# Optimization experiments

Measured on AMD Instinct MI355X. Metric: run time of the kernel, lower is better.

Reference implementation:

```python
import jax, jax.numpy as jnp
import numpy as np

B, L, DIM, NH = 2, 2048, 1024, 16
HD = DIM // NH

def setup_inputs() -> dict:
    key = jax.random.key(0)
    ks = jax.random.split(key, 7)
    s = 1.0 / np.sqrt(DIM)
    x = jax.random.normal(ks[0], (B, L, DIM), dtype=jnp.float32)
    pos_bias = jax.random.normal(ks[1], (B, NH, L, L), dtype=jnp.float32)
    mask = jax.random.randint(ks[2], (B, L), 0, 2, dtype=jnp.int32)
    wq = jax.random.normal(ks[3], (DIM, DIM), dtype=jnp.float32) * s
    wk = jax.random.normal(ks[4], (DIM, DIM), dtype=jnp.float32) * s
    wv = jax.random.normal(ks[5], (DIM, DIM), dtype=jnp.float32) * s
    wo = jax.random.normal(ks[6], (DIM, DIM), dtype=jnp.float32) * s
    return {"x": x, "pos_bias": pos_bias, "mask": mask, "wq": wq, "wk": wk, "wv": wv, "wo": wo}

def reference(x, pos_bias, mask, wq, wk, wv, wo):
    b, l, _ = x.shape
    # projections (bias-free linears); reshape to [B, L, n, c]
    q = (x @ wq).reshape(b, l, NH, HD)
    k = (x @ wk).reshape(b, l, NH, HD)
    v = (x @ wv).reshape(b, l, NH, HD)
    # additive bias: pos_bias, with masked positions set to dtype min (T5: no 1/sqrt(d) scaling)
    neg = jnp.finfo(x.dtype).min
    attn_bias = jnp.where(mask[:, None, None, :] == 0, neg, pos_bias)
    scores = jnp.einsum('binc,bjnc->bnij', q, k) + attn_bias  # [B, n, L, L]
    attn = jax.nn.softmax(scores, axis=-1)
    out = jnp.einsum('bnij,bjnc->binc', attn, v).reshape(b, l, DIM)
    return out @ wo
```

## Files before the change

### kernel.cpp

```cpp
#include <hip/hip_runtime.h>
#include <cmath>

typedef _Float16 half8 __attribute__((ext_vector_type(8)));
typedef _Float16 half4 __attribute__((ext_vector_type(4)));
typedef float f32x4 __attribute__((ext_vector_type(4)));

#define NEGBIG (-3.4028235e38f)

__global__ void cast4_kernel(const float* __restrict__ in, _Float16* __restrict__ out, int n) {
    int i = (blockIdx.x * 256 + threadIdx.x) * 4;
    if (i < n) {
        float4 v = *(const float4*)&in[i];
        half4 o = { (_Float16)v.x, (_Float16)v.y, (_Float16)v.z, (_Float16)v.w };
        *(half4*)&out[i] = o;
    }
}

__global__ void transpose_cast_kernel(const float* __restrict__ W, _Float16* __restrict__ Wt) {
    __shared__ float tile[32][33];
    int bx = blockIdx.x * 32;
    int by = blockIdx.y * 32;
    int tx = threadIdx.x & 31, ty = threadIdx.x >> 5;
    #pragma unroll
    for (int r = 0; r < 32; r += 8)
        tile[ty + r][tx] = W[(size_t)(bx + ty + r) * 1024 + by + tx];
    __syncthreads();
    #pragma unroll
    for (int r = 0; r < 32; r += 8)
        Wt[(size_t)(by + ty + r) * 1024 + bx + tx] = (_Float16)tile[tx][ty + r];
}

__global__ __launch_bounds__(256)
void gemm_qkv_kernel(const _Float16* __restrict__ X,
                     const _Float16* __restrict__ WqT, const _Float16* __restrict__ WkT,
                     const _Float16* __restrict__ WvT,
                     _Float16* __restrict__ Qh, _Float16* __restrict__ Kh, _Float16* __restrict__ VTh)
{
    const int z = blockIdx.z;
    const _Float16* __restrict__ Bt = (z == 0) ? WqT : (z == 1) ? WkT : WvT;
    _Float16* __restrict__ out      = (z == 0) ? Qh  : (z == 1) ? Kh  : VTh;

    __shared__ _Float16 Asb[128][40];
    __shared__ _Float16 Bsb[128][40];

    const int tid = threadIdx.x;
    const int bm = blockIdx.x * 128;
    const int bn = blockIdx.y * 128;
    const int wave = tid >> 6, lane = tid & 63;
    const int wm = (wave >> 1) * 64, wn = (wave & 1) * 64;
    const int quad = lane >> 4, l16 = lane & 15;

    f32x4 acc[4][4] = {};

    for (int k0 = 0; k0 < 1024; k0 += 32) {
        #pragma unroll
        for (int c = 0; c < 2; ++c) {
            int chunk = tid + c * 256;
            int row = chunk >> 2;
            int kc  = (chunk & 3) * 8;
            *(half8*)&Asb[row][kc] = *(const half8*)&X [(size_t)(bm + row) * 1024 + k0 + kc];
            *(half8*)&Bsb[row][kc] = *(const half8*)&Bt[(size_t)(bn + row) * 1024 + k0 + kc];
        }
        __syncthreads();
        half8 af[4], bf[4];
        #pragma unroll
        for (int mt = 0; mt < 4; ++mt) af[mt] = *(const half8*)&Asb[wm + mt*16 + l16][quad * 8];
        #pragma unroll
        for (int nt = 0; nt < 4; ++nt) bf[nt] = *(const half8*)&Bsb[wn + nt*16 + l16][quad * 8];
        #pragma unroll
        for (int mt = 0; mt < 4; ++mt)
            #pragma unroll
            for (int nt = 0; nt < 4; ++nt)
                acc[mt][nt] = __builtin_amdgcn_mfma_f32_16x16x32_f16(af[mt], bf[nt], acc[mt][nt], 0, 0, 0);
        __syncthreads();
    }

    #pragma unroll
    for (int mt = 0; mt < 4; ++mt) {
        #pragma unroll
        for (int nt = 0; nt < 4; ++nt) {
            #pragma unroll
            for (int r = 0; r < 4; ++r) {
                int m = bm + wm + mt * 16 + quad * 4 + r;
                int n = bn + wn + nt * 16 + l16;
                _Float16 hv = (_Float16)acc[mt][nt][r];
                int bb = m >> 11, ll = m & 2047, hh = n >> 6, dd = n & 63;
                if (z < 2)
                    out[(((size_t)(bb * 16 + hh)) * 2048 + ll) * 64 + dd] = hv;
                else
                    out[(((size_t)(bb * 16 + hh)) * 64 + dd) * 2048 + ll] = hv;
            }
        }
    }
}

__device__ __forceinline__ float rowmax16(float v) {
    #pragma unroll
    for (int off = 1; off < 16; off <<= 1) v = fmaxf(v, __shfl_xor(v, off));
    return v;
}
__device__ __forceinline__ float rowsum16(float v) {
    #pragma unroll
    for (int off = 1; off < 16; off <<= 1) v += __shfl_xor(v, off);
    return v;
}

__global__ __launch_bounds__(256)
void flash_attn_kernel(const _Float16* __restrict__ Qh, const _Float16* __restrict__ Kh,
                       const _Float16* __restrict__ VTh, const float* __restrict__ bias,
                       const int* __restrict__ mask, _Float16* __restrict__ AO)
{
    const int qt = blockIdx.x, h = blockIdx.y, b = blockIdx.z;
    const int tid = threadIdx.x, wave = tid >> 6, lane = tid & 63;
    const int quad = lane >> 4, l16 = lane & 15;

    __shared__ _Float16 Kt[64][72];
    __shared__ _Float16 Vt[64][72];
    __shared__ _Float16 Pw[4][16][72];

    const size_t head = (size_t)(b * 16 + h) * 2048 * 64;
    const int i_base = qt * 64 + wave * 16;
    const int ig0 = i_base + quad * 4;

    half8 qf0 = *(const half8*)&Qh[head + (size_t)(i_base + l16) * 64 + quad * 8];
    half8 qf1 = *(const half8*)&Qh[head + (size_t)(i_base + l16) * 64 + 32 + quad * 8];

    float m_r[4] = { -INFINITY, -INFINITY, -INFINITY, -INFINITY };
    float l_r[4] = {};
    f32x4 o[4] = {};

    for (int j0 = 0; j0 < 2048; j0 += 64) {
        #pragma unroll
        for (int c = 0; c < 2; ++c) {
            int chunk = tid + c * 256;
            int row = chunk >> 3;
            int dc  = (chunk & 7) * 8;
            *(half8*)&Kt[row][dc] = *(const half8*)&Kh [head + (size_t)(j0 + row) * 64 + dc];
            *(half8*)&Vt[row][dc] = *(const half8*)&VTh[head + (size_t)row * 2048 + j0 + dc];
        }
        __syncthreads();

        float sreg[4][4];
        #pragma unroll
        for (int jt = 0; jt < 4; ++jt) {
            half8 kf0 = *(const half8*)&Kt[jt * 16 + l16][quad * 8];
            half8 kf1 = *(const half8*)&Kt[jt * 16 + l16][32 + quad * 8];
            f32x4 s = {};
            s = __builtin_amdgcn_mfma_f32_16x16x32_f16(qf0, kf0, s, 0, 0, 0);
            s = __builtin_amdgcn_mfma_f32_16x16x32_f16(qf1, kf1, s, 0, 0, 0);
            int jg = j0 + jt * 16 + l16;
            int mv = mask[b * 2048 + jg];
            const float* bp = bias + ((size_t)((b * 16 + h) * 2048 + ig0)) * 2048 + jg;
            #pragma unroll
            for (int r = 0; r < 4; ++r) {
                float bv = bp[(size_t)r * 2048];
                sreg[jt][r] = s[r] + (mv ? bv : NEGBIG);
            }
        }

        float alpha[4];
        #pragma unroll
        for (int r = 0; r < 4; ++r) {
            float mx = fmaxf(fmaxf(sreg[0][r], sreg[1][r]), fmaxf(sreg[2][r], sreg[3][r]));
            mx = rowmax16(mx);
            float mnew = fmaxf(m_r[r], mx);
            alpha[r] = __expf(m_r[r] - mnew);
            m_r[r] = mnew;
            float ps = 0.f;
            #pragma unroll
            for (int jt = 0; jt < 4; ++jt) {
                float p = __expf(sreg[jt][r] - mnew);
                Pw[wave][quad * 4 + r][jt * 16 + l16] = (_Float16)p;
                ps += p;
            }
            ps = rowsum16(ps);
            l_r[r] = l_r[r] * alpha[r] + ps;
        }
        #pragma unroll
        for (int nt = 0; nt < 4; ++nt)
            #pragma unroll
            for (int r = 0; r < 4; ++r)
                o[nt][r] *= alpha[r];

        half8 pf0 = *(const half8*)&Pw[wave][l16][quad * 8];
        half8 pf1 = *(const half8*)&Pw[wave][l16][32 + quad * 8];
        #pragma unroll
        for (int nt = 0; nt < 4; ++nt) {
            half8 vf0 = *(const half8*)&Vt[nt * 16 + l16][quad * 8];
            half8 vf1 = *(const half8*)&Vt[nt * 16 + l16][32 + quad * 8];
            o[nt] = __builtin_amdgcn_mfma_f32_16x16x32_f16(pf0, vf0, o[nt], 0, 0, 0);
            o[nt] = __builtin_amdgcn_mfma_f32_16x16x32_f16(pf1, vf1, o[nt], 0, 0, 0);
        }
        __syncthreads();
    }

    #pragma unroll
    for (int nt = 0; nt < 4; ++nt) {
        #pragma unroll
        for (int r = 0; r < 4; ++r) {
            float val = o[nt][r] / l_r[r];
            AO[(size_t)(b * 2048 + i_base + quad * 4 + r) * 1024 + h * 64 + nt * 16 + l16] = (_Float16)val;
        }
    }
}

__global__ __launch_bounds__(256)
void gemm_out_kernel(const _Float16* __restrict__ A, const _Float16* __restrict__ Bt,
                     float* __restrict__ C)
{
    __shared__ _Float16 Asb[128][40];
    __shared__ _Float16 Bsb[128][40];

    const int tid = threadIdx.x;
    const int bm = blockIdx.x * 128;
    const int bn = blockIdx.y * 128;
    const int wave = tid >> 6, lane = tid & 63;
    const int wm = (wave >> 1) * 64, wn = (wave & 1) * 64;
    const int quad = lane >> 4, l16 = lane & 15;

    f32x4 acc[4][4] = {};

    for (int k0 = 0; k0 < 1024; k0 += 32) {
        #pragma unroll
        for (int c = 0; c < 2; ++c) {
            int chunk = tid + c * 256;
            int row = chunk >> 2;
            int kc  = (chunk & 3) * 8;
            *(half8*)&Asb[row][kc] = *(const half8*)&A [(size_t)(bm + row) * 1024 + k0 + kc];
            *(half8*)&Bsb[row][kc] = *(const half8*)&Bt[(size_t)(bn + row) * 1024 + k0 + kc];
        }
        __syncthreads();
        half8 af[4], bf[4];
        #pragma unroll
        for (int mt = 0; mt < 4; ++mt) af[mt] = *(const half8*)&Asb[wm + mt*16 + l16][quad * 8];
        #pragma unroll
        for (int nt = 0; nt < 4; ++nt) bf[nt] = *(const half8*)&Bsb[wn + nt*16 + l16][quad * 8];
        #pragma unroll
        for (int mt = 0; mt < 4; ++mt)
            #pragma unroll
            for (int nt = 0; nt < 4; ++nt)
                acc[mt][nt] = __builtin_amdgcn_mfma_f32_16x16x32_f16(af[mt], bf[nt], acc[mt][nt], 0, 0, 0);
        __syncthreads();
    }

    #pragma unroll
    for (int mt = 0; mt < 4; ++mt)
        #pragma unroll
        for (int nt = 0; nt < 4; ++nt)
            #pragma unroll
            for (int r = 0; r < 4; ++r) {
                int m = bm + wm + mt * 16 + quad * 4 + r;
                int n = bn + wn + nt * 16 + l16;
                C[(size_t)m * 1024 + n] = acc[mt][nt][r];
            }
}

extern "C" void kernel_launch(void* const* d_in, const int* in_sizes, int n_in,
                              void* d_out, int out_size, void* d_ws, size_t ws_size,
                              hipStream_t stream)
{
    const float* x    = (const float*)d_in[0];
    const float* bias = (const float*)d_in[1];
    const int*   mask = (const int*)d_in[2];
    const float* wq   = (const float*)d_in[3];
    const float* wk   = (const float*)d_in[4];
    const float* wv   = (const float*)d_in[5];
    const float* wo   = (const float*)d_in[6];
    float* out = (float*)d_out;

    char* ws = (char*)d_ws;
    const size_t MB = 1024 * 1024;
    _Float16* x_h = (_Float16*)(ws + 0);
    _Float16* AO  = x_h;
    _Float16* wqT = (_Float16*)(ws + 8 * MB);
    _Float16* wkT = (_Float16*)(ws + 10 * MB);
    _Float16* wvT = (_Float16*)(ws + 12 * MB);
    _Float16* woT = (_Float16*)(ws + 14 * MB);
    _Float16* Qh  = (_Float16*)(ws + 16 * MB);
    _Float16* Kh  = (_Float16*)(ws + 24 * MB);
    _Float16* VTh = (_Float16*)(ws + 32 * MB);

    cast4_kernel<<<4096, 256, 0, stream>>>(x, x_h, 4096 * 1024);
    dim3 tg(32, 32);
    transpose_cast_kernel<<<tg, 256, 0, stream>>>(wq, wqT);
    transpose_cast_kernel<<<tg, 256, 0, stream>>>(wk, wkT);
    transpose_cast_kernel<<<tg, 256, 0, stream>>>(wv, wvT);
    transpose_cast_kernel<<<tg, 256, 0, stream>>>(wo, woT);

    gemm_qkv_kernel<<<dim3(32, 8, 3), 256, 0, stream>>>(x_h, wqT, wkT, wvT, Qh, Kh, VTh);
    flash_attn_kernel<<<dim3(32, 16, 2), 256, 0, stream>>>(Qh, Kh, VTh, bias, mask, AO);
    gemm_out_kernel<<<dim3(32, 8), 256, 0, stream>>>(AO, woT, out);
}
```

Before: 830.4 us.

## Use async global-to-LDS loads, stage bias tiles, coalesce QKV stores

Replaces the register-staged global loads in both GEMMs and the attention K/V loads with direct global-to-LDS async loads, and widens the GEMM k-step to 64. The attention kernel now loads and masks the pos_bias tile with coalesced float4 reads into shared memory, prefetching the next tile into registers, instead of doing scattered scalar bias and mask reads per MFMA fragment. The QKV GEMM epilogue goes through an LDS transpose buffer so Q, K and V^T are written as 16-byte vectors. The unpadded 64-wide LDS rows may cause bank conflicts on fragment reads, and the async loads are only separated from their use by __syncthreads.

```diff
diff --git a/kernel.cpp b/kernel.cpp
--- a/kernel.cpp
+++ b/kernel.cpp
@@ -1,11 +1,18 @@
 #include <hip/hip_runtime.h>
 #include <cmath>
+#include <cstdint>
 
 typedef _Float16 half8 __attribute__((ext_vector_type(8)));
 typedef _Float16 half4 __attribute__((ext_vector_type(4)));
 typedef float f32x4 __attribute__((ext_vector_type(4)));
 
 #define NEGBIG (-3.4028235e38f)
+
+__device__ __forceinline__ void async16(const void* g, void* l) {
+    __builtin_amdgcn_global_load_lds(
+        (const __attribute__((address_space(1))) uint32_t*)g,
+        (__attribute__((address_space(3))) uint32_t*)l, 16, 0, 0);
+}
 
 __global__ void cast4_kernel(const float* __restrict__ in, _Float16* __restrict__ out, int n) {
     int i = (blockIdx.x * 256 + threadIdx.x) * 4;
@@ -36,60 +43,74 @@
                      const _Float16* __restrict__ WvT,
                      _Float16* __restrict__ Qh, _Float16* __restrict__ Kh, _Float16* __restrict__ VTh)
 {
+    __shared__ __align__(16) char smem_raw[34816];
+    _Float16* Alds = (_Float16*)smem_raw;
+    _Float16* Blds = Alds + 8192;
+    typedef _Float16 CtRow[136];
+    CtRow* Ct = (CtRow*)smem_raw;
+
     const int z = blockIdx.z;
     const _Float16* __restrict__ Bt = (z == 0) ? WqT : (z == 1) ? WkT : WvT;
-    _Float16* __restrict__ out      = (z == 0) ? Qh  : (z == 1) ? Kh  : VTh;
-
-    __shared__ _Float16 Asb[128][40];
-    __shared__ _Float16 Bsb[128][40];
 
     const int tid = threadIdx.x;
-    const int bm = blockIdx.x * 128;
-    const int bn = blockIdx.y * 128;
+    const int bm = blockIdx.x * 128, bn = blockIdx.y * 128;
     const int wave = tid >> 6, lane = tid & 63;
     const int wm = (wave >> 1) * 64, wn = (wave & 1) * 64;
     const int quad = lane >> 4, l16 = lane & 15;
 
     f32x4 acc[4][4] = {};
 
-    for (int k0 = 0; k0 < 1024; k0 += 32) {
-        #pragma unroll
-        for (int c = 0; c < 2; ++c) {
-            int chunk = tid + c * 256;
-            int row = chunk >> 2;
-            int kc  = (chunk & 3) * 8;
-            *(half8*)&Asb[row][kc] = *(const half8*)&X [(size_t)(bm + row) * 1024 + k0 + kc];
-            *(half8*)&Bsb[row][kc] = *(const half8*)&Bt[(size_t)(bn + row) * 1024 + k0 + kc];
-        }
-        __syncthreads();
-        half8 af[4], bf[4];
-        #pragma unroll
-        for (int mt = 0; mt < 4; ++mt) af[mt] = *(const half8*)&Asb[wm + mt*16 + l16][quad * 8];
-        #pragma unroll
-        for (int nt = 0; nt < 4; ++nt) bf[nt] = *(const half8*)&Bsb[wn + nt*16 + l16][quad * 8];
-        #pragma unroll
-        for (int mt = 0; mt < 4; ++mt)
-            #pragma unroll
-            for (int nt = 0; nt < 4; ++nt)
-                acc[mt][nt] = __builtin_amdgcn_mfma_f32_16x16x32_f16(af[mt], bf[nt], acc[mt][nt], 0, 0, 0);
-        __syncthreads();
-    }
-
-    #pragma unroll
-    for (int mt = 0; mt < 4; ++mt) {
-        #pragma unroll
-        for (int nt = 0; nt < 4; ++nt) {
+    for (int k0 = 0; k0 < 1024; k0 += 64) {
+        #pragma unroll
+        for (int t = 0; t < 4; ++t) {
+            int s = t * 256 + tid;
+            int row = s >> 3, kc = (s & 7) * 8;
+            async16(&X [(size_t)(bm + row) * 1024 + k0 + kc], &Alds[s * 8]);
+            async16(&Bt[(size_t)(bn + row) * 1024 + k0 + kc], &Blds[s * 8]);
+        }
+        __syncthreads();
+        #pragma unroll
+        for (int kk = 0; kk < 64; kk += 32) {
+            half8 af[4], bf[4];
+            #pragma unroll
+            for (int mt = 0; mt < 4; ++mt) af[mt] = *(const half8*)&Alds[(wm + mt*16 + l16) * 64 + kk + quad * 8];
+            #pragma unroll
+            for (int nt = 0; nt < 4; ++nt) bf[nt] = *(const half8*)&Blds[(wn + nt*16 + l16) * 64 + kk + quad * 8];
+            #pragma unroll
+            for (int mt = 0; mt < 4; ++mt)
+                #pragma unroll
+                for (int nt = 0; nt < 4; ++nt)
+                    acc[mt][nt] = __builtin_amdgcn_mfma_f32_16x16x32_f16(af[mt], bf[nt], acc[mt][nt], 0, 0, 0);
+        }
+        __syncthreads();
+    }
+
+    #pragma unroll
+    for (int mt = 0; mt < 4; ++mt)
+        #pragma unroll
+        for (int nt = 0; nt < 4; ++nt)
             #pragma unroll
             for (int r = 0; r < 4; ++r) {
-                int m = bm + wm + mt * 16 + quad * 4 + r;
-                int n = bn + wn + nt * 16 + l16;
+                int row = wm + mt * 16 + quad * 4 + r;
+                int col = wn + nt * 16 + l16;
                 _Float16 hv = (_Float16)acc[mt][nt][r];
-                int bb = m >> 11, ll = m & 2047, hh = n >> 6, dd = n & 63;
-                if (z < 2)
-                    out[(((size_t)(bb * 16 + hh)) * 2048 + ll) * 64 + dd] = hv;
-                else
-                    out[(((size_t)(bb * 16 + hh)) * 64 + dd) * 2048 + ll] = hv;
+                if (z < 2) Ct[row][col] = hv; else Ct[col][row] = hv;
             }
+    __syncthreads();
+
+    const int bb = bm >> 11, lbase = bm & 2047;
+    _Float16* __restrict__ outQK = (z == 0) ? Qh : Kh;
+    #pragma unroll
+    for (int step = 0; step < 8; ++step) {
+        int r  = step * 16 + (tid >> 4);
+        int c8 = (tid & 15) * 8;
+        half8 v = *(const half8*)&Ct[r][c8];
+        if (z < 2) {
+            int n = bn + c8, hh = n >> 6, dd = n & 63;
+            *(half8*)&outQK[(((size_t)(bb * 16 + hh)) * 2048 + (lbase + r)) * 64 + dd] = v;
+        } else {
+            int n = bn + r, hh = n >> 6, dd = n & 63;
+            *(half8*)&VTh[(((size_t)(bb * 16 + hh)) * 64 + dd) * 2048 + lbase + c8] = v;
         }
     }
 }
@@ -114,13 +135,14 @@
     const int tid = threadIdx.x, wave = tid >> 6, lane = tid & 63;
     const int quad = lane >> 4, l16 = lane & 15;
 
-    __shared__ _Float16 Kt[64][72];
-    __shared__ _Float16 Vt[64][72];
+    __shared__ __align__(16) _Float16 Kt[64 * 64];
+    __shared__ __align__(16) _Float16 Vt[64 * 64];
     __shared__ _Float16 Pw[4][16][72];
+    __shared__ float    Bs[64][66];
 
     const size_t head = (size_t)(b * 16 + h) * 2048 * 64;
     const int i_base = qt * 64 + wave * 16;
-    const int ig0 = i_base + quad * 4;
+    const size_t bias_base = ((size_t)((b * 16 + h) * 2048 + qt * 64)) * 2048;
 
     half8 qf0 = *(const half8*)&Qh[head + (size_t)(i_base + l16) * 64 + quad * 8];
     half8 qf1 = *(const half8*)&Qh[head + (size_t)(i_base + l16) * 64 + 32 + quad * 8];
@@ -129,33 +151,53 @@
     float l_r[4] = {};
     f32x4 o[4] = {};
 
+    float4 bpre[4]; int4 mpre[4];
+    #pragma unroll
+    for (int p = 0; p < 4; ++p) {
+        int s = p * 256 + tid; int il = s >> 4; int jc = (s & 15) * 4;
+        bpre[p] = *(const float4*)&bias[bias_base + (size_t)il * 2048 + jc];
+        mpre[p] = *(const int4*)&mask[b * 2048 + jc];
+    }
+
     for (int j0 = 0; j0 < 2048; j0 += 64) {
         #pragma unroll
         for (int c = 0; c < 2; ++c) {
-            int chunk = tid + c * 256;
-            int row = chunk >> 3;
-            int dc  = (chunk & 7) * 8;
-            *(half8*)&Kt[row][dc] = *(const half8*)&Kh [head + (size_t)(j0 + row) * 64 + dc];
-            *(half8*)&Vt[row][dc] = *(const half8*)&VTh[head + (size_t)row * 2048 + j0 + dc];
-        }
-        __syncthreads();
+            int s = c * 256 + tid;
+            int row = s >> 3, dc = (s & 7) * 8;
+            async16(&Kh [head + (size_t)(j0 + row) * 64 + dc], &Kt[s * 8]);
+            async16(&VTh[head + (size_t)row * 2048 + j0 + dc], &Vt[s * 8]);
+        }
+        #pragma unroll
+        for (int p = 0; p < 4; ++p) {
+            int s = p * 256 + tid; int il = s >> 4; int jc = (s & 15) * 4;
+            float4 v = bpre[p]; int4 mv = mpre[p];
+            Bs[il][jc + 0] = mv.x ? v.x : NEGBIG;
+            Bs[il][jc + 1] = mv.y ? v.y : NEGBIG;
+            Bs[il][jc + 2] = mv.z ? v.z : NEGBIG;
+            Bs[il][jc + 3] = mv.w ? v.w : NEGBIG;
+        }
+        __syncthreads();
+
+        if (j0 + 64 < 2048) {
+            #pragma unroll
+            for (int p = 0; p < 4; ++p) {
+                int s = p * 256 + tid; int il = s >> 4; int jc = (s & 15) * 4;
+                bpre[p] = *(const float4*)&bias[bias_base + (size_t)il * 2048 + j0 + 64 + jc];
+                mpre[p] = *(const int4*)&mask[b * 2048 + j0 + 64 + jc];
+            }
+        }
 
         float sreg[4][4];
         #pragma unroll
         for (int jt = 0; jt < 4; ++jt) {
-            half8 kf0 = *(const half8*)&Kt[jt * 16 + l16][quad * 8];
-            half8 kf1 = *(const half8*)&Kt[jt * 16 + l16][32 + quad * 8];
+            half8 kf0 = *(const half8*)&Kt[(jt * 16 + l16) * 64 + quad * 8];
+            half8 kf1 = *(const half8*)&Kt[(jt * 16 + l16) * 64 + 32 + quad * 8];
             f32x4 s = {};
             s = __builtin_amdgcn_mfma_f32_16x16x32_f16(qf0, kf0, s, 0, 0, 0);
             s = __builtin_amdgcn_mfma_f32_16x16x32_f16(qf1, kf1, s, 0, 0, 0);
-            int jg = j0 + jt * 16 + l16;
-            int mv = mask[b * 2048 + jg];
-            const float* bp = bias + ((size_t)((b * 16 + h) * 2048 + ig0)) * 2048 + jg;
-            #pragma unroll
-            for (int r = 0; r < 4; ++r) {
-                float bv = bp[(size_t)r * 2048];
-                sreg[jt][r] = s[r] + (mv ? bv : NEGBIG);
-            }
+            #pragma unroll
+            for (int r = 0; r < 4; ++r)
+                sreg[jt][r] = s[r] + Bs[wave * 16 + quad * 4 + r][jt * 16 + l16];
         }
 
         float alpha[4];
@@ -186,8 +228,8 @@
         half8 pf1 = *(const half8*)&Pw[wave][l16][32 + quad * 8];
         #pragma unroll
         for (int nt = 0; nt < 4; ++nt) {
-            half8 vf0 = *(const half8*)&Vt[nt * 16 + l16][quad * 8];
-            half8 vf1 = *(const half8*)&Vt[nt * 16 + l16][32 + quad * 8];
+            half8 vf0 = *(const half8*)&Vt[(nt * 16 + l16) * 64 + quad * 8];
+            half8 vf1 = *(const half8*)&Vt[(nt * 16 + l16) * 64 + 32 + quad * 8];
             o[nt] = __builtin_amdgcn_mfma_f32_16x16x32_f16(pf0, vf0, o[nt], 0, 0, 0);
             o[nt] = __builtin_amdgcn_mfma_f32_16x16x32_f16(pf1, vf1, o[nt], 0, 0, 0);
         }
@@ -208,38 +250,39 @@
 void gemm_out_kernel(const _Float16* __restrict__ A, const _Float16* __restrict__ Bt,
                      float* __restrict__ C)
 {
-    __shared__ _Float16 Asb[128][40];
-    __shared__ _Float16 Bsb[128][40];
+    __shared__ __align__(16) _Float16 Alds[8192];
+    __shared__ __align__(16) _Float16 Blds[8192];
 
     const int tid = threadIdx.x;
-    const int bm = blockIdx.x * 128;
-    const int bn = blockIdx.y * 128;
+    const int bm = blockIdx.x * 128, bn = blockIdx.y * 128;
     const int wave = tid >> 6, lane = tid & 63;
     const int wm = (wave >> 1) * 64, wn = (wave & 1) * 64;
     const int quad = lane >> 4, l16 = lane & 15;
 
     f32x4 acc[4][4] = {};
 
-    for (int k0 = 0; k0 < 1024; k0 += 32) {
-        #pragma unroll
-        for (int c = 0; c < 2; ++c) {
-            int chunk = tid + c * 256;
-            int row = chunk >> 2;
-            int kc  = (chunk & 3) * 8;
-            *(half8*)&Asb[row][kc] = *(const half8*)&A [(size_t)(bm + row) * 1024 + k0 + kc];
-            *(half8*)&Bsb[row][kc] = *(const half8*)&Bt[(size_t)(bn + row) * 1024 + k0 + kc];
-        }
-        __syncthreads();
-        half8 af[4], bf[4];
-        #pragma unroll
-        for (int mt = 0; mt < 4; ++mt) af[mt] = *(const half8*)&Asb[wm + mt*16 + l16][quad * 8];
-        #pragma unroll
-        for (int nt = 0; nt < 4; ++nt) bf[nt] = *(const half8*)&Bsb[wn + nt*16 + l16][quad * 8];
-        #pragma unroll
-        for (int mt = 0; mt < 4; ++mt)
-            #pragma unroll
-            for (int nt = 0; nt < 4; ++nt)
-                acc[mt][nt] = __builtin_amdgcn_mfma_f32_16x16x32_f16(af[mt], bf[nt], acc[mt][nt], 0, 0, 0);
+    for (int k0 = 0; k0 < 1024; k0 += 64) {
+        #pragma unroll
+        for (int t = 0; t < 4; ++t) {
+            int s = t * 256 + tid;
+            int row = s >> 3, kc = (s & 7) * 8;
+            async16(&A [(size_t)(bm + row) * 1024 + k0 + kc], &Alds[s * 8]);
+            async16(&Bt[(size_t)(bn + row) * 1024 + k0 + kc], &Blds[s * 8]);
+        }
+        __syncthreads();
+        #pragma unroll
+        for (int kk = 0; kk < 64; kk += 32) {
+            half8 af[4], bf[4];
+            #pragma unroll
+            for (int mt = 0; mt < 4; ++mt) af[mt] = *(const half8*)&Alds[(wm + mt*16 + l16) * 64 + kk + quad * 8];
+            #pragma unroll
+            for (int nt = 0; nt < 4; ++nt) bf[nt] = *(const half8*)&Blds[(wn + nt*16 + l16) * 64 + kk + quad * 8];
+            #pragma unroll
+            for (int mt = 0; mt < 4; ++mt)
+                #pragma unroll
+                for (int nt = 0; nt < 4; ++nt)
+                    acc[mt][nt] = __builtin_amdgcn_mfma_f32_16x16x32_f16(af[mt], bf[nt], acc[mt][nt], 0, 0, 0);
+        }
         __syncthreads();
     }
 
```

Result: slower. 887.8 us (+6.9%).
